# Kernel optimization log

Measured on AMD Instinct MI355X. Metric: run time of the kernel, lower is better.

The kernel has to match this reference:

```python
import jax, jax.numpy as jnp
import numpy as np

CH_J = 64      # number of output capsules
N_J = 32       # output capsule dim
R_NUM = 3      # routing iterations
B_ALPHAS = (8.0, 8.0, 8.0)
EPS = 1e-7     # K.epsilon()


def _squeeze(s):
    # squash nonlinearity: |s|^2/(1+|s|^2) * s/|s|
    sq = jnp.sum(s * s, axis=-1, keepdims=True)
    return (sq / (1.0 + sq)) * (s * jax.lax.rsqrt(sq + EPS))


def setup_inputs() -> dict:
    key = jax.random.key(0)
    k1, k2 = jax.random.split(key)
    B, CH_I, N_I = 16, 2048, 16
    inputs = jax.random.normal(k1, (B, CH_I, N_I), dtype=jnp.float32)
    # glorot-ish scale for the transform kernel (ch_i, n_i, ch_j, n_j)
    w = jax.random.normal(k2, (CH_I, N_I, CH_J, N_J), dtype=jnp.float32) * 0.05
    return {"inputs": inputs, "w": w}


def reference(inputs, w):
    # prediction vectors u[b,i,j,m] = sum_n inputs[b,i,n] * w[i,n,j,m]
    u = jnp.einsum('bin,injm->bijm', inputs, w)
    u_sg = jax.lax.stop_gradient(u)
    b = jnp.zeros(u.shape[:3], dtype=u.dtype)  # (B, ch_i, ch_j) routing logits
    v = None
    for r in range(R_NUM):
        if r > 0:
            c = jax.lax.stop_gradient(
                jax.nn.softmax(b * B_ALPHAS[r], axis=-1))[..., None] * CH_J
        else:
            c = 1.0
        ub = u if r == R_NUM - 1 else u_sg
        s = jnp.sum(c * ub, axis=1)  # (B, ch_j, n_j)
        v = _squeeze(s)
        if r == R_NUM - 1:
            break
        v = jax.lax.stop_gradient(v)
        # agreement update: a[b,i,j] = sum_m v[b,j,m] * u[b,i,j,m]
        b = b + jnp.einsum('bjm,bijm->bij', v, u)
    return v  # (B, ch_j, n_j)
```

## Files before the change

### kernel.cpp

```cpp
#include <hip/hip_runtime.h>
#include <hip/hip_fp16.h>
#include <math.h>

#define B_   16
#define CI   2048
#define NI   16
#define CJ   64
#define NJ   32
#define JM   2048
#define CH   8
#define NCH  256
#define ALPHA 8.0f

template <int PASS, bool ATOMIC, bool STOREU>
__global__ __launch_bounds__(1024)
void pass_kernel(const float* __restrict__ x, const float* __restrict__ w,
                 const float* __restrict__ vprev, float* __restrict__ a0,
                 float* __restrict__ sout, __half* __restrict__ U16)
{
    __shared__ float xs[CH][8][NI];
    __shared__ float Ls[8][CJ];
    __shared__ float smax[8], sinv[8];

    const int idx    = blockIdx.x;
    const int xcd    = idx & 7;
    const int bhalf  = (idx >> 3) & 1;
    const int slot   = idx >> 4;
    const int ichunk = slot * 8 + xcd;
    const int i0     = ichunk * CH;
    const int b0     = bhalf * 8;

    const int tid  = threadIdx.x;
    const int bh   = tid >> 8;
    const int jg   = tid & 255;
    const int jm0  = jg * 8;
    const int jcol = jg >> 2;

    if (tid < 256) {
        const int f  = tid * 4;
        const int n  = f & 15;
        const int bg = (f >> 4) & 7;
        const int ci = f >> 7;
        *(float4*)(&xs[ci][bg][n]) =
            *(const float4*)(x + ((size_t)(b0 + bg) * CI + (i0 + ci)) * NI + n);
    }

    float acc[2][8];
#pragma unroll
    for (int bb = 0; bb < 2; ++bb)
#pragma unroll
        for (int k = 0; k < 8; ++k) acc[bb][k] = 0.0f;

    __syncthreads();

    for (int ci = 0; ci < CH; ++ci) {
        const int i = i0 + ci;

        float u[2][8];
#pragma unroll
        for (int bb = 0; bb < 2; ++bb)
#pragma unroll
            for (int k = 0; k < 8; ++k) u[bb][k] = 0.0f;

        const float* wrow = w + (size_t)i * (NI * JM) + jm0;
#pragma unroll
        for (int n = 0; n < NI; ++n) {
            const float4 w0 = *(const float4*)(wrow + (size_t)n * JM);
            const float4 w1 = *(const float4*)(wrow + (size_t)n * JM + 4);
#pragma unroll
            for (int bb = 0; bb < 2; ++bb) {
                const float xv = xs[ci][bh * 2 + bb][n];
                u[bb][0] = fmaf(xv, w0.x, u[bb][0]);
                u[bb][1] = fmaf(xv, w0.y, u[bb][1]);
                u[bb][2] = fmaf(xv, w0.z, u[bb][2]);
                u[bb][3] = fmaf(xv, w0.w, u[bb][3]);
                u[bb][4] = fmaf(xv, w1.x, u[bb][4]);
                u[bb][5] = fmaf(xv, w1.y, u[bb][5]);
                u[bb][6] = fmaf(xv, w1.z, u[bb][6]);
                u[bb][7] = fmaf(xv, w1.w, u[bb][7]);
            }
        }

        if (PASS == 0) {
#pragma unroll
            for (int bb = 0; bb < 2; ++bb)
#pragma unroll
                for (int k = 0; k < 8; ++k) acc[bb][k] += u[bb][k];
            if (STOREU) {
#pragma unroll
                for (int bb = 0; bb < 2; ++bb) {
                    const int b = b0 + bh * 2 + bb;
                    union { uint4 q; __half h[8]; } pk;
#pragma unroll
                    for (int k = 0; k < 8; ++k) pk.h[k] = __float2half(u[bb][k]);
                    *(uint4*)(U16 + ((size_t)b * CI + i) * JM + jm0) = pk.q;
                }
            }
        } else {
            float ap[2];
#pragma unroll
            for (int bb = 0; bb < 2; ++bb) {
                const int b = b0 + bh * 2 + bb;
                const float4 v0 = *(const float4*)(vprev + (size_t)b * JM + jm0);
                const float4 v1 = *(const float4*)(vprev + (size_t)b * JM + jm0 + 4);
                float t = u[bb][0] * v0.x + u[bb][1] * v0.y
                        + u[bb][2] * v0.z + u[bb][3] * v0.w
                        + u[bb][4] * v1.x + u[bb][5] * v1.y
                        + u[bb][6] * v1.z + u[bb][7] * v1.w;
                t += __shfl_xor(t, 1);
                t += __shfl_xor(t, 2);
                ap[bb] = t;
            }

            float L[2];
#pragma unroll
            for (int bb = 0; bb < 2; ++bb) {
                if (PASS == 1) {
                    L[bb] = ap[bb];
                } else {
                    const int b = b0 + bh * 2 + bb;
                    L[bb] = ap[bb] + a0[((size_t)b * CI + i) * CJ + jcol];
                }
            }
            if ((jg & 3) == 0) {
#pragma unroll
                for (int bb = 0; bb < 2; ++bb) {
                    const int bg = bh * 2 + bb;
                    Ls[bg][jcol] = L[bb];
                    if (PASS == 1)
                        a0[((size_t)(b0 + bg) * CI + i) * CJ + jcol] = ap[bb];
                }
            }
            __syncthreads();

            if (tid < 256) {
                const int rb = tid >> 5, rj = tid & 31;
                const float x1 = Ls[rb][rj];
                const float x2 = Ls[rb][rj + 32];
                float mx = fmaxf(x1, x2);
#pragma unroll
                for (int s2 = 1; s2 < 32; s2 <<= 1)
                    mx = fmaxf(mx, __shfl_xor(mx, s2));
                float ex = __expf(ALPHA * (x1 - mx)) + __expf(ALPHA * (x2 - mx));
#pragma unroll
                for (int s2 = 1; s2 < 32; s2 <<= 1)
                    ex += __shfl_xor(ex, s2);
                if (rj == 0) { smax[rb] = mx; sinv[rb] = 64.0f / ex; }
            }
            __syncthreads();

#pragma unroll
            for (int bb = 0; bb < 2; ++bb) {
                const int bg = bh * 2 + bb;
                const float c = __expf(ALPHA * (L[bb] - smax[bg])) * sinv[bg];
#pragma unroll
                for (int k = 0; k < 8; ++k)
                    acc[bb][k] = fmaf(c, u[bb][k], acc[bb][k]);
            }
        }
    }

    if (ATOMIC) {
#pragma unroll
        for (int bb = 0; bb < 2; ++bb) {
            const int b = b0 + bh * 2 + bb;
#pragma unroll
            for (int k = 0; k < 8; ++k)
                unsafeAtomicAdd(sout + (size_t)b * JM + jm0 + k, acc[bb][k]);
        }
    } else {
#pragma unroll
        for (int bb = 0; bb < 2; ++bb) {
            const int b = b0 + bh * 2 + bb;
            float* dst = sout + ((size_t)b * NCH + ichunk) * JM + jm0;
            *(float4*)(dst)     =
                make_float4(acc[bb][0], acc[bb][1], acc[bb][2], acc[bb][3]);
            *(float4*)(dst + 4) =
                make_float4(acc[bb][4], acc[bb][5], acc[bb][6], acc[bb][7]);
        }
    }
}

template <int PASS>
__global__ __launch_bounds__(256)
void route_kernel(const __half* __restrict__ U16, const float* __restrict__ vprev,
                  float* __restrict__ a0, float* __restrict__ part)
{
    __shared__ float vT[32 * 64];

    const int tid = threadIdx.x;
    const int b   = blockIdx.x >> 6;
    const int ig  = blockIdx.x & 63;
    const int wv  = tid >> 6;
    const int l   = tid & 63;

    {
        const float* vp = vprev + (size_t)b * JM + tid * 8;
        const float4 f0 = *(const float4*)(vp);
        const float4 f1 = *(const float4*)(vp + 4);
        const float tmp[8] = {f0.x, f0.y, f0.z, f0.w, f1.x, f1.y, f1.z, f1.w};
#pragma unroll
        for (int k = 0; k < 8; ++k) {
            const int jm = tid * 8 + k;
            vT[(jm & 31) * 64 + (jm >> 5)] = tmp[k];
        }
    }
    __syncthreads();

    float acc[32];
#pragma unroll
    for (int m = 0; m < 32; ++m) acc[m] = 0.0f;

    for (int ii = 0; ii < 8; ++ii) {
        const int i = ig * 32 + wv * 8 + ii;
        const __half* up = U16 + ((size_t)b * CI + i) * JM + l * 32;

        union { float4 f; __half2 h2[4]; } r[4];
        r[0].f = *(const float4*)(up);
        r[1].f = *(const float4*)(up + 8);
        r[2].f = *(const float4*)(up + 16);
        r[3].f = *(const float4*)(up + 24);

        float ap = 0.0f;
#pragma unroll
        for (int q = 0; q < 4; ++q)
#pragma unroll
            for (int p = 0; p < 4; ++p) {
                const float2 w2 = __half22float2(r[q].h2[p]);
                const int m = q * 8 + p * 2;
                ap = fmaf(vT[m * 64 + l], w2.x, ap);
                ap = fmaf(vT[(m + 1) * 64 + l], w2.y, ap);
            }

        float L = ap;
        if (PASS == 2)
            L += a0[((size_t)b * CI + i) * CJ + l];
        if (PASS == 1)
            a0[((size_t)b * CI + i) * CJ + l] = ap;

        float mx = L;
#pragma unroll
        for (int d = 1; d < 64; d <<= 1)
            mx = fmaxf(mx, __shfl_xor(mx, d));
        const float e = __expf(ALPHA * (L - mx));
        float se = e;
#pragma unroll
        for (int d = 1; d < 64; d <<= 1)
            se += __shfl_xor(se, d);
        const float c = e * (64.0f / se);

#pragma unroll
        for (int q = 0; q < 4; ++q)
#pragma unroll
            for (int p = 0; p < 4; ++p) {
                const float2 w2 = __half22float2(r[q].h2[p]);
                const int m = q * 8 + p * 2;
                acc[m]     = fmaf(c, w2.x, acc[m]);
                acc[m + 1] = fmaf(c, w2.y, acc[m + 1]);
            }
    }

    float* dst = part + ((size_t)b * NCH + (ig * 4 + wv)) * JM + l * 32;
#pragma unroll
    for (int q = 0; q < 8; ++q)
        *(float4*)(dst + q * 4) =
            make_float4(acc[q * 4], acc[q * 4 + 1], acc[q * 4 + 2], acc[q * 4 + 3]);
}

__global__ __launch_bounds__(1024)
void reduce_squash(const float* __restrict__ part, float* __restrict__ v)
{
    __shared__ float red[4][256];
    const int tid = threadIdx.x;
    const int seg = tid >> 8;
    const int loc = tid & 255;
    const int b   = blockIdx.x >> 3;
    const int jmb = (blockIdx.x & 7) * 256;

    const float* p = part + ((size_t)b * NCH + seg * 64) * JM + jmb + loc;
    float s0 = 0.f, s1 = 0.f, s2 = 0.f, s3 = 0.f;
#pragma unroll 4
    for (int q = 0; q < 64; q += 4) {
        s0 += p[(size_t)(q + 0) * JM];
        s1 += p[(size_t)(q + 1) * JM];
        s2 += p[(size_t)(q + 2) * JM];
        s3 += p[(size_t)(q + 3) * JM];
    }
    red[seg][loc] = (s0 + s1) + (s2 + s3);
    __syncthreads();

    if (tid < 256) {
        const float s = (red[0][loc] + red[1][loc]) + (red[2][loc] + red[3][loc]);
        float sq = s * s;
#pragma unroll
        for (int k = 1; k < 32; k <<= 1) sq += __shfl_xor(sq, k);
        v[(size_t)b * JM + jmb + loc] =
            (sq / (1.0f + sq)) * (s * rsqrtf(sq + 1e-7f));
    }
}

__global__ __launch_bounds__(256)
void squash_kernel(const float* __restrict__ s, float* __restrict__ v)
{
    const int g = blockIdx.x * 256 + threadIdx.x;
    const float val = s[g];
    float sq = val * val;
#pragma unroll
    for (int k = 1; k < 32; k <<= 1) sq += __shfl_xor(sq, k);
    v[g] = (sq / (1.0f + sq)) * (val * rsqrtf(sq + 1e-7f));
}

extern "C" void kernel_launch(void* const* d_in, const int* in_sizes, int n_in,
                              void* d_out, int out_size, void* d_ws, size_t ws_size,
                              hipStream_t stream)
{
    const float* x = (const float*)d_in[0];
    const float* w = (const float*)d_in[1];
    float* out = (float*)d_out;
    float* ws  = (float*)d_ws;

    float* A0   = ws;
    float* V0   = A0 + (size_t)B_ * CI * CJ;
    float* V1   = V0 + (size_t)B_ * JM;
    float* PART = V1 + (size_t)B_ * JM;
    __half* U16 = (__half*)(PART + (size_t)B_ * NCH * JM);

    const size_t need_part =
        ((size_t)B_ * CI * CJ + 2 * (size_t)B_ * JM
         + (size_t)B_ * NCH * JM) * sizeof(float);
    const size_t need_full =
        need_part + (size_t)B_ * CI * JM * sizeof(__half);

    if (ws_size >= need_full) {
        pass_kernel<0, false, true><<<512, 1024, 0, stream>>>(x, w, nullptr, nullptr, PART, U16);
        reduce_squash<<<128, 1024, 0, stream>>>(PART, V0);
        route_kernel<1><<<1024, 256, 0, stream>>>(U16, V0, A0, PART);
        reduce_squash<<<128, 1024, 0, stream>>>(PART, V1);
        route_kernel<2><<<1024, 256, 0, stream>>>(U16, V1, A0, PART);
        reduce_squash<<<128, 1024, 0, stream>>>(PART, out);
    } else if (ws_size >= need_part) {
        pass_kernel<0, false, false><<<512, 1024, 0, stream>>>(x, w, nullptr, nullptr, PART, nullptr);
        reduce_squash<<<128, 1024, 0, stream>>>(PART, V0);
        pass_kernel<1, false, false><<<512, 1024, 0, stream>>>(x, w, V0, A0, PART, nullptr);
        reduce_squash<<<128, 1024, 0, stream>>>(PART, V1);
        pass_kernel<2, false, false><<<512, 1024, 0, stream>>>(x, w, V1, A0, PART, nullptr);
        reduce_squash<<<128, 1024, 0, stream>>>(PART, out);
    } else {
        float* S0 = V1 + (size_t)B_ * JM;
        float* S1 = S0 + (size_t)B_ * JM;
        float* S2 = S1 + (size_t)B_ * JM;
        hipMemsetAsync(S0, 0, (size_t)3 * B_ * JM * sizeof(float), stream);
        pass_kernel<0, true, false><<<512, 1024, 0, stream>>>(x, w, nullptr, nullptr, S0, nullptr);
        squash_kernel<<<128, 256, 0, stream>>>(S0, V0);
        pass_kernel<1, true, false><<<512, 1024, 0, stream>>>(x, w, V0, A0, S1, nullptr);
        squash_kernel<<<128, 256, 0, stream>>>(S1, V1);
        pass_kernel<2, true, false><<<512, 1024, 0, stream>>>(x, w, V1, A0, S2, nullptr);
        squash_kernel<<<128, 256, 0, stream>>>(S2, out);
    }
}
```

Measured before the change: 585.1 us.

## Fold routing logits into summed v, fuse batch in pass0, prefetch U rows

Drops the stored routing-logit array A0 in the fast path. The last iteration's logits are recomputed as the dot of u with (v0+v1), which is exact by linearity of the agreement update, so a0 is neither written nor read. Pass 0 gets a dedicated kernel where each block covers all 16 batches for an i-chunk, so each w slice is read once instead of twice. The route kernel keeps v in registers instead of a transposed LDS copy and prefetches the next U row in registers, adding register pressure in exchange for removing LDS traffic and a sync.

```diff
diff --git a/kernel.cpp b/kernel.cpp
--- a/kernel.cpp
+++ b/kernel.cpp
@@ -11,6 +11,87 @@
 #define CH   8
 #define NCH  256
 #define ALPHA 8.0f
+
+__global__ __launch_bounds__(1024)
+void pass0_full(const float* __restrict__ x, const float* __restrict__ w,
+                float* __restrict__ part, __half* __restrict__ U16)
+{
+    __shared__ float xs[CH][16][NI];
+
+    const int ichunk = blockIdx.x;
+    const int i0     = ichunk * CH;
+    const int tid    = threadIdx.x;
+    const int bh     = tid >> 8;
+    const int jg     = tid & 255;
+    const int jm0    = jg * 8;
+
+    if (tid < 512) {
+        const int f  = tid * 4;
+        const int n  = f & 15;
+        const int b  = (f >> 4) & 15;
+        const int ci = f >> 8;
+        *(float4*)(&xs[ci][b][n]) =
+            *(const float4*)(x + ((size_t)b * CI + (i0 + ci)) * NI + n);
+    }
+
+    float acc[4][8];
+#pragma unroll
+    for (int bb = 0; bb < 4; ++bb)
+#pragma unroll
+        for (int k = 0; k < 8; ++k) acc[bb][k] = 0.0f;
+
+    __syncthreads();
+
+    for (int ci = 0; ci < CH; ++ci) {
+        const int i = i0 + ci;
+
+        float u[4][8];
+#pragma unroll
+        for (int bb = 0; bb < 4; ++bb)
+#pragma unroll
+            for (int k = 0; k < 8; ++k) u[bb][k] = 0.0f;
+
+        const float* wrow = w + (size_t)i * (NI * JM) + jm0;
+#pragma unroll
+        for (int n = 0; n < NI; ++n) {
+            const float4 w0 = *(const float4*)(wrow + (size_t)n * JM);
+            const float4 w1 = *(const float4*)(wrow + (size_t)n * JM + 4);
+#pragma unroll
+            for (int bb = 0; bb < 4; ++bb) {
+                const float xv = xs[ci][bh * 4 + bb][n];
+                u[bb][0] = fmaf(xv, w0.x, u[bb][0]);
+                u[bb][1] = fmaf(xv, w0.y, u[bb][1]);
+                u[bb][2] = fmaf(xv, w0.z, u[bb][2]);
+                u[bb][3] = fmaf(xv, w0.w, u[bb][3]);
+                u[bb][4] = fmaf(xv, w1.x, u[bb][4]);
+                u[bb][5] = fmaf(xv, w1.y, u[bb][5]);
+                u[bb][6] = fmaf(xv, w1.z, u[bb][6]);
+                u[bb][7] = fmaf(xv, w1.w, u[bb][7]);
+            }
+        }
+
+#pragma unroll
+        for (int bb = 0; bb < 4; ++bb) {
+#pragma unroll
+            for (int k = 0; k < 8; ++k) acc[bb][k] += u[bb][k];
+            const int b = bh * 4 + bb;
+            union { uint4 q; __half h[8]; } pk;
+#pragma unroll
+            for (int k = 0; k < 8; ++k) pk.h[k] = __float2half(u[bb][k]);
+            *(uint4*)(U16 + ((size_t)b * CI + i) * JM + jm0) = pk.q;
+        }
+    }
+
+#pragma unroll
+    for (int bb = 0; bb < 4; ++bb) {
+        const int b = bh * 4 + bb;
+        float* dst = part + ((size_t)b * NCH + ichunk) * JM + jm0;
+        *(float4*)(dst)     =
+            make_float4(acc[bb][0], acc[bb][1], acc[bb][2], acc[bb][3]);
+        *(float4*)(dst + 4) =
+            make_float4(acc[bb][4], acc[bb][5], acc[bb][6], acc[bb][7]);
+    }
+}
 
 template <int PASS, bool ATOMIC, bool STOREU>
 __global__ __launch_bounds__(1024)
@@ -181,68 +262,70 @@
     }
 }
 
-template <int PASS>
+template <bool TWO>
 __global__ __launch_bounds__(256)
-void route_kernel(const __half* __restrict__ U16, const float* __restrict__ vprev,
-                  float* __restrict__ a0, float* __restrict__ part)
-{
-    __shared__ float vT[32 * 64];
-
+void route_kernel(const __half* __restrict__ U16, const float* __restrict__ va,
+                  const float* __restrict__ vb, float* __restrict__ part)
+{
     const int tid = threadIdx.x;
     const int b   = blockIdx.x >> 6;
     const int ig  = blockIdx.x & 63;
     const int wv  = tid >> 6;
     const int l   = tid & 63;
 
-    {
-        const float* vp = vprev + (size_t)b * JM + tid * 8;
-        const float4 f0 = *(const float4*)(vp);
-        const float4 f1 = *(const float4*)(vp + 4);
-        const float tmp[8] = {f0.x, f0.y, f0.z, f0.w, f1.x, f1.y, f1.z, f1.w};
-#pragma unroll
-        for (int k = 0; k < 8; ++k) {
-            const int jm = tid * 8 + k;
-            vT[(jm & 31) * 64 + (jm >> 5)] = tmp[k];
-        }
-    }
-    __syncthreads();
+    float vr[32];
+#pragma unroll
+    for (int q = 0; q < 8; ++q) {
+        const float4 f = *(const float4*)(va + (size_t)b * JM + l * 32 + q * 4);
+        vr[q * 4 + 0] = f.x; vr[q * 4 + 1] = f.y;
+        vr[q * 4 + 2] = f.z; vr[q * 4 + 3] = f.w;
+    }
+    if (TWO) {
+#pragma unroll
+        for (int q = 0; q < 8; ++q) {
+            const float4 f = *(const float4*)(vb + (size_t)b * JM + l * 32 + q * 4);
+            vr[q * 4 + 0] += f.x; vr[q * 4 + 1] += f.y;
+            vr[q * 4 + 2] += f.z; vr[q * 4 + 3] += f.w;
+        }
+    }
 
     float acc[32];
 #pragma unroll
     for (int m = 0; m < 32; ++m) acc[m] = 0.0f;
 
+    const __half* up0 = U16 + ((size_t)b * CI + ig * 32 + wv * 8) * JM + l * 32;
+
+    union F4H { float4 f; __half2 h2[4]; };
+    F4H cur[4], nxt[4];
+#pragma unroll
+    for (int q = 0; q < 4; ++q)
+        cur[q].f = *(const float4*)(up0 + q * 8);
+
+#pragma unroll
     for (int ii = 0; ii < 8; ++ii) {
-        const int i = ig * 32 + wv * 8 + ii;
-        const __half* up = U16 + ((size_t)b * CI + i) * JM + l * 32;
-
-        union { float4 f; __half2 h2[4]; } r[4];
-        r[0].f = *(const float4*)(up);
-        r[1].f = *(const float4*)(up + 8);
-        r[2].f = *(const float4*)(up + 16);
-        r[3].f = *(const float4*)(up + 24);
+        if (ii < 7) {
+            const __half* upn = up0 + (size_t)(ii + 1) * JM;
+#pragma unroll
+            for (int q = 0; q < 4; ++q)
+                nxt[q].f = *(const float4*)(upn + q * 8);
+        }
 
         float ap = 0.0f;
 #pragma unroll
         for (int q = 0; q < 4; ++q)
 #pragma unroll
             for (int p = 0; p < 4; ++p) {
-                const float2 w2 = __half22float2(r[q].h2[p]);
+                const float2 uf = __half22float2(cur[q].h2[p]);
                 const int m = q * 8 + p * 2;
-                ap = fmaf(vT[m * 64 + l], w2.x, ap);
-                ap = fmaf(vT[(m + 1) * 64 + l], w2.y, ap);
-            }
-
-        float L = ap;
-        if (PASS == 2)
-            L += a0[((size_t)b * CI + i) * CJ + l];
-        if (PASS == 1)
-            a0[((size_t)b * CI + i) * CJ + l] = ap;
-
-        float mx = L;
+                ap = fmaf(vr[m],     uf.x, ap);
+                ap = fmaf(vr[m + 1], uf.y, ap);
+            }
+
+        float mx = ap;
 #pragma unroll
         for (int d = 1; d < 64; d <<= 1)
             mx = fmaxf(mx, __shfl_xor(mx, d));
-        const float e = __expf(ALPHA * (L - mx));
+        const float e = __expf(ALPHA * (ap - mx));
         float se = e;
 #pragma unroll
         for (int d = 1; d < 64; d <<= 1)
@@ -253,11 +336,14 @@
         for (int q = 0; q < 4; ++q)
 #pragma unroll
             for (int p = 0; p < 4; ++p) {
-                const float2 w2 = __half22float2(r[q].h2[p]);
+                const float2 uf = __half22float2(cur[q].h2[p]);
                 const int m = q * 8 + p * 2;
-                acc[m]     = fmaf(c, w2.x, acc[m]);
-                acc[m + 1] = fmaf(c, w2.y, acc[m + 1]);
-            }
+                acc[m]     = fmaf(c, uf.x, acc[m]);
+                acc[m + 1] = fmaf(c, uf.y, acc[m + 1]);
+            }
+
+#pragma unroll
+        for (int q = 0; q < 4; ++q) cur[q] = nxt[q];
     }
 
     float* dst = part + ((size_t)b * NCH + (ig * 4 + wv)) * JM + l * 32;
@@ -332,11 +418,11 @@
         need_part + (size_t)B_ * CI * JM * sizeof(__half);
 
     if (ws_size >= need_full) {
-        pass_kernel<0, false, true><<<512, 1024, 0, stream>>>(x, w, nullptr, nullptr, PART, U16);
+        pass0_full<<<256, 1024, 0, stream>>>(x, w, PART, U16);
         reduce_squash<<<128, 1024, 0, stream>>>(PART, V0);
-        route_kernel<1><<<1024, 256, 0, stream>>>(U16, V0, A0, PART);
+        route_kernel<false><<<1024, 256, 0, stream>>>(U16, V0, nullptr, PART);
         reduce_squash<<<128, 1024, 0, stream>>>(PART, V1);
-        route_kernel<2><<<1024, 256, 0, stream>>>(U16, V1, A0, PART);
+        route_kernel<true><<<1024, 256, 0, stream>>>(U16, V0, V1, PART);
         reduce_squash<<<128, 1024, 0, stream>>>(PART, out);
     } else if (ws_size >= need_part) {
         pass_kernel<0, false, false><<<512, 1024, 0, stream>>>(x, w, nullptr, nullptr, PART, nullptr);
```

Measured after the change: 547.5 us. 1.07x faster.
